# Kernel optimization log

Hardware: AMD Instinct MI355X
Metric: run time of the kernel (lower is better)

Reference implementation:

```python
import jax, jax.numpy as jnp
import numpy as np

D_MODEL = 1024
N_HEADS = 16
D_HEAD = D_MODEL // N_HEADS
LN_EPS = 1e-5


def setup_inputs() -> dict:
    key = jax.random.key(0)
    ks = jax.random.split(key, 8)
    B, T = 4, 2048
    s = 1.0 / np.sqrt(D_MODEL)
    return {
        "encoder_seq": jax.random.normal(ks[0], (B, T, D_MODEL), jnp.float32),
        "decoder_seq": jax.random.normal(ks[1], (B, T, D_MODEL), jnp.float32),
        "Wq": jax.random.normal(ks[2], (D_MODEL, D_MODEL), jnp.float32) * s,
        "bq": jnp.zeros((D_MODEL,), jnp.float32),
        "Wk": jax.random.normal(ks[3], (D_MODEL, D_MODEL), jnp.float32) * s,
        "bk": jnp.zeros((D_MODEL,), jnp.float32),
        "Wv": jax.random.normal(ks[4], (D_MODEL, D_MODEL), jnp.float32) * s,
        "bv": jnp.zeros((D_MODEL,), jnp.float32),
        "ln_gamma": jnp.ones((D_MODEL,), jnp.float32),
        "ln_beta": jnp.zeros((D_MODEL,), jnp.float32),
    }


def layer_norm(x, gamma, beta):
    mu = jnp.mean(x, axis=-1, keepdims=True)
    var = jnp.mean(jnp.square(x - mu), axis=-1, keepdims=True)
    return (x - mu) * jax.lax.rsqrt(var + LN_EPS) * gamma + beta


def reference(encoder_seq, decoder_seq, Wq, bq, Wk, bk, Wv, bv, ln_gamma, ln_beta):
    B, T_dec, _ = decoder_seq.shape
    T_enc = encoder_seq.shape[1]
    # projections (torch Linear: x @ W^T + b)
    q = (decoder_seq @ Wq.T + bq).reshape(B, T_dec, N_HEADS, D_HEAD)
    k = (encoder_seq @ Wk.T + bk).reshape(B, T_enc, N_HEADS, D_HEAD)
    v = (encoder_seq @ Wv.T + bv).reshape(B, T_enc, N_HEADS, D_HEAD)
    scale = 1.0 / np.sqrt(D_HEAD)
    # softmax-free attention: scale*(Q K^T) V == scale * Q (K^T V); avoid [T_dec,T_enc]
    kv = jnp.einsum("bthd,bthe->bhde", k, v)          # [B,H,dh,dh]
    att = jnp.einsum("bqhd,bhde->bqhe", q, kv) * scale  # [B,T_dec,H,dh]
    att = att.reshape(B, T_dec, D_MODEL)
    # dropout is identity in eval mode; residual + LayerNorm
    return layer_norm(att + decoder_seq, ln_gamma, ln_beta)
```

## Files before the change

### kernel.cpp

```cpp
#include <hip/hip_runtime.h>
#include <hip/hip_bf16.h>
#include <stdint.h>
#include <stddef.h>

typedef __attribute__((ext_vector_type(8))) __bf16 bf16x8;
typedef __attribute__((ext_vector_type(4))) float f32x4;

#define DMODEL 1024
#define HEADS  16
#define BATCH  4
#define TSEQ   2048
#define MROWS  (BATCH * TSEQ)
#define NE     (MROWS * DMODEL)
#define NW     (DMODEL * DMODEL)

#define MiB (size_t)1048576
#define QB_OFF   ((size_t)0)
#define KB_OFF   (16 * MiB)
#define VB_OFF   (32 * MiB)
#define ENC_OFF  (48 * MiB)
#define DEC_OFF  (64 * MiB)
#define KVP_OFF  (64 * MiB)
#define WB_OFF   (80 * MiB)
#define KVT_OFF  (86 * MiB)

__global__ __launch_bounds__(256)
void conv_all(const float* __restrict__ enc, const float* __restrict__ dec,
              const float* __restrict__ Wq, const float* __restrict__ Wk,
              const float* __restrict__ Wv,
              __bf16* __restrict__ encB, __bf16* __restrict__ decB,
              __bf16* __restrict__ WB)
{
    const int i = (blockIdx.x * 256 + threadIdx.x) * 8;
    const float* src;
    __bf16* dst;
    int off;
    if (i < NE)            { src = enc; dst = encB; off = i; }
    else if (i < 2 * NE)   { src = dec; dst = decB; off = i - NE; }
    else {
        const int j = i - 2 * NE;
        const int sel = j >> 20;
        off = j & (NW - 1);
        src = (sel == 0) ? Wq : (sel == 1) ? Wk : Wv;
        dst = WB + (size_t)sel * NW;
    }
    f32x4 a = *(const f32x4*)(src + off);
    f32x4 b = *(const f32x4*)(src + off + 4);
    bf16x8 o;
#pragma unroll
    for (int j = 0; j < 4; ++j) { o[j] = (__bf16)a[j]; o[j + 4] = (__bf16)b[j]; }
    *(bf16x8*)(dst + off) = o;
}

__device__ __forceinline__ bf16x8 frag(const __bf16* reg, int rowl, int kh, int g4)
{
    const int slot = ((kh << 2) + g4) ^ (rowl & 7);
    return *(const bf16x8*)(reg + rowl * 64 + slot * 8);
}

__device__ __forceinline__ void stage_half(const __bf16* gbase, int kt,
                                           __bf16* reg, int tid)
{
#pragma unroll
    for (int p = 0; p < 2; ++p) {
        const int c = tid + p * 512;
        const int row = c >> 3, slot = c & 7;
        const __bf16* src = gbase + (size_t)row * DMODEL + kt * 64
                            + ((slot ^ (row & 7)) << 3);
        __builtin_amdgcn_global_load_lds(
            (const __attribute__((address_space(1))) void*)src,
            (__attribute__((address_space(3))) void*)(reg + c * 8), 16, 0, 0);
    }
}

#define VMW(N)  asm volatile("s_waitcnt vmcnt(" #N ")" ::: "memory")
#define LGKM0() asm volatile("s_waitcnt lgkmcnt(0)" ::: "memory")

#define KPHASE(PAR, STAGE_CODE, WAIT_CODE)                                    \
  {                                                                           \
    bf16x8 af[4][2], bfv[4][2];                                               \
    _Pragma("unroll") for (int mf = 0; mf < 4; ++mf)                          \
      _Pragma("unroll") for (int kh = 0; kh < 2; ++kh)                        \
        af[mf][kh] = frag(&ldsA[PAR][0], wm * 64 + mf * 16 + l4, kh, g4);     \
    _Pragma("unroll") for (int nf = 0; nf < 4; ++nf)                          \
      _Pragma("unroll") for (int kh = 0; kh < 2; ++kh)                        \
        bfv[nf][kh] = frag(&ldsB[PAR][bh][0], (wn & 1) * 64 + nf * 16 + l4, kh, g4); \
    LGKM0();                                                                  \
    __builtin_amdgcn_sched_barrier(0);                                        \
    __builtin_amdgcn_s_barrier();        \
    STAGE_CODE;                      \
    __builtin_amdgcn_sched_barrier(0);                                        \
    __builtin_amdgcn_s_setprio(1);                                            \
    _Pragma("unroll") for (int mf = 0; mf < 4; ++mf)                          \
      _Pragma("unroll") for (int nf = 0; nf < 4; ++nf)                        \
        _Pragma("unroll") for (int kh = 0; kh < 2; ++kh)                      \
          acc[mf][nf] = __builtin_amdgcn_mfma_f32_16x16x32_bf16(              \
              af[mf][kh], bfv[nf][kh], acc[mf][nf], 0, 0, 0);                 \
    __builtin_amdgcn_s_setprio(0);                                            \
    WAIT_CODE;                                                                \
    __builtin_amdgcn_s_barrier();    \
  }

__global__ __launch_bounds__(512, 2)
void qkv_gemm(const __bf16* __restrict__ decB, const __bf16* __restrict__ encB,
              const __bf16* __restrict__ WB,
              const float* __restrict__ bq, const float* __restrict__ bk,
              const float* __restrict__ bv,
              __bf16* __restrict__ Qb, __bf16* __restrict__ Kb,
              __bf16* __restrict__ Vb)
{
    __shared__ __align__(16) __bf16 ldsA[2][8192];
    __shared__ __align__(16) __bf16 ldsB[2][2][8192];

    const int tid  = threadIdx.x;
    const int lane = tid & 63;
    const int wv   = tid >> 6;
    const int wm   = wv >> 2;
    const int wn   = wv & 3;
    const int bh   = wn >> 1;
    const int l4   = lane & 15;
    const int g4   = lane >> 4;

    const int bid  = blockIdx.x;
    const int slab = bid & 7;
    const int idx  = bid >> 3;
    const int r    = idx >> 3;
    const int sel  = r >> 2;
    const int bn   = r & 3;
    const int bm   = slab * 8 + (idx & 7);

    const __bf16* A    = (sel == 0) ? decB : encB;
    const __bf16* W    = WB + (size_t)sel * NW;
    const float*  bias = (sel == 0) ? bq : (sel == 1) ? bk : bv;
    __bf16*       C    = (sel == 0) ? Qb : (sel == 1) ? Kb : Vb;

    const __bf16* Ab = A + (size_t)(bm * 128) * DMODEL;
    const __bf16* Wb = W + (size_t)(bn * 256) * DMODEL;

    auto stage_tile = [&](int par, int kt) {
        stage_half(Ab,                        kt, &ldsA[par][0],    tid);
        stage_half(Wb,                        kt, &ldsB[par][0][0], tid);
        stage_half(Wb + (size_t)128 * DMODEL, kt, &ldsB[par][1][0], tid);
    };

    f32x4 acc[4][4] = {};

    stage_tile(0, 0);
    stage_tile(1, 1);
    VMW(6);
    __builtin_amdgcn_s_barrier();

    for (int i = 0; i < 8; ++i) {
        KPHASE(0, { if (i < 7) stage_tile(0, 2 * i + 2); },
                  { if (i < 7) { VMW(6); } else { VMW(0); } })
        KPHASE(1, { if (i < 7) stage_tile(1, 2 * i + 3); },
                  { if (i < 7) { VMW(6); } else { VMW(0); } })
    }

#pragma unroll
    for (int mf = 0; mf < 4; ++mf)
#pragma unroll
        for (int nf = 0; nf < 4; ++nf) {
            const int gm0 = bm * 128 + wm * 64 + mf * 16 + g4 * 4;
            const int gn  = bn * 256 + wn * 64 + nf * 16 + l4;
            const float bv2 = bias[gn];
#pragma unroll
            for (int j = 0; j < 4; ++j)
                C[(size_t)(gm0 + j) * DMODEL + gn] =
                    (__bf16)(acc[mf][nf][j] + bv2);
        }
}

__global__ __launch_bounds__(256)
void kv_mm(const __bf16* __restrict__ Kb, const __bf16* __restrict__ Vb,
           float* __restrict__ kvp)
{
    __shared__ __align__(16) float Ks[128][64];
    __shared__ __align__(16) float Vs[128][64];

    const int tid = threadIdx.x;
    const int bh  = blockIdx.x;
    const int ch  = blockIdx.y;
    const int b   = bh >> 4, h = bh & 15;
    const int w   = tid >> 6, lane = tid & 63;
    const int dg  = (lane >> 3) * 8;
    const int eg  = (lane & 7) * 8;
    const size_t base = (size_t)b * TSEQ + (size_t)ch * 512;

    f32x4 acc[8][2] = {};

    for (int ss = 0; ss < 4; ++ss) {
        __syncthreads();
#pragma unroll
        for (int i = 0; i < 4; ++i) {
            const int e = i * 2048 + tid * 8;
            const int t = e >> 6, d = e & 63;
            bf16x8 k8 = *(const bf16x8*)&Kb[(base + ss * 128 + t) * DMODEL + h * 64 + d];
            bf16x8 v8 = *(const bf16x8*)&Vb[(base + ss * 128 + t) * DMODEL + h * 64 + d];
            f32x4 kf0, kf1, vf0, vf1;
#pragma unroll
            for (int j = 0; j < 4; ++j) {
                kf0[j] = (float)k8[j]; kf1[j] = (float)k8[j + 4];
                vf0[j] = (float)v8[j]; vf1[j] = (float)v8[j + 4];
            }
            *(f32x4*)&Ks[t][d]     = kf0;
            *(f32x4*)&Ks[t][d + 4] = kf1;
            *(f32x4*)&Vs[t][d]     = vf0;
            *(f32x4*)&Vs[t][d + 4] = vf1;
        }
        __syncthreads();

#pragma unroll 4
        for (int tt = 0; tt < 32; ++tt) {
            const int t = w * 32 + tt;
            f32x4 kd0 = *(const f32x4*)&Ks[t][dg];
            f32x4 kd1 = *(const f32x4*)&Ks[t][dg + 4];
            f32x4 ve0 = *(const f32x4*)&Vs[t][eg];
            f32x4 ve1 = *(const f32x4*)&Vs[t][eg + 4];
#pragma unroll
            for (int rr = 0; rr < 8; ++rr) {
                const float kd = (rr < 4) ? kd0[rr] : kd1[rr - 4];
                acc[rr][0] += ve0 * kd;
                acc[rr][1] += ve1 * kd;
            }
        }
    }

    float* o = kvp + ((size_t)(ch * 4 + w) * 64 + bh) * 4096 + (size_t)dg * 64 + eg;
#pragma unroll
    for (int rr = 0; rr < 8; ++rr) {
        *(f32x4*)(o + rr * 64)     = acc[rr][0];
        *(f32x4*)(o + rr * 64 + 4) = acc[rr][1];
    }
}

__global__ __launch_bounds__(256)
void kv_reduce(const float* __restrict__ kvp, __bf16* __restrict__ kvT)
{
    const int idx = blockIdx.x * 256 + threadIdx.x;
    const int bh  = idx >> 12;
    const int rem = idx & 4095;
    const int d = rem >> 6, e = rem & 63;
    float s = 0.f;
#pragma unroll
    for (int c = 0; c < 16; ++c) s += kvp[((size_t)c * 64 + bh) * 4096 + rem];
    kvT[(size_t)bh * 4096 + e * 64 + d] = (__bf16)(s * 0.125f);
}

__global__ __launch_bounds__(256)
void att_ln(const __bf16* __restrict__ Q, const __bf16* __restrict__ kvT,
            const float* __restrict__ dec, const float* __restrict__ gamma,
            const float* __restrict__ beta, float* __restrict__ out)
{
    __shared__ __align__(16) __bf16 att_s[32][1032];

    const int tid  = threadIdx.x;
    const int lane = tid & 63;
    const int w    = tid >> 6;
    const int l4   = lane & 15, g4 = lane >> 4;
    const int t0   = blockIdx.x * 32;
    const int b    = t0 >> 11;

#pragma unroll
    for (int i = 0; i < 4; ++i) {
        const int h = w * 4 + i;
        f32x4 acc[2][4] = {};
#pragma unroll
        for (int kk = 0; kk < 2; ++kk) {
            bf16x8 a0 = *(const bf16x8*)&Q[(size_t)(t0 + l4) * DMODEL + h * 64 + kk * 32 + g4 * 8];
            bf16x8 a1 = *(const bf16x8*)&Q[(size_t)(t0 + 16 + l4) * DMODEL + h * 64 + kk * 32 + g4 * 8];
#pragma unroll
            for (int n = 0; n < 4; ++n) {
                bf16x8 bb = *(const bf16x8*)&kvT[(size_t)(b * 16 + h) * 4096 + (n * 16 + l4) * 64 + kk * 32 + g4 * 8];
                acc[0][n] = __builtin_amdgcn_mfma_f32_16x16x32_bf16(a0, bb, acc[0][n], 0, 0, 0);
                acc[1][n] = __builtin_amdgcn_mfma_f32_16x16x32_bf16(a1, bb, acc[1][n], 0, 0, 0);
            }
        }
#pragma unroll
        for (int m = 0; m < 2; ++m)
#pragma unroll
            for (int n = 0; n < 4; ++n)
#pragma unroll
                for (int j = 0; j < 4; ++j)
                    att_s[m * 16 + g4 * 4 + j][h * 64 + n * 16 + l4] = (__bf16)acc[m][n][j];
    }
    __syncthreads();

    const int rr = tid >> 3, seg = tid & 7;
    const size_t grow = (size_t)t0 + rr;
    float sum = 0.f, ss2 = 0.f;
#pragma unroll
    for (int i = 0; i < 16; ++i) {
        const int c0 = seg * 8 + i * 64;
        bf16x8 av = *(const bf16x8*)&att_s[rr][c0];
        f32x4 d0 = *(const f32x4*)&dec[grow * DMODEL + c0];
        f32x4 d1 = *(const f32x4*)&dec[grow * DMODEL + c0 + 4];
        bf16x8 xs;
#pragma unroll
        for (int j = 0; j < 4; ++j) {
            const float x0 = (float)av[j] + d0[j];
            const float x1 = (float)av[j + 4] + d1[j];
            sum += x0 + x1; ss2 += x0 * x0 + x1 * x1;
            xs[j] = (__bf16)x0; xs[j + 4] = (__bf16)x1;
        }
        *(bf16x8*)&att_s[rr][c0] = xs;
    }
    sum += __shfl_xor(sum, 1); ss2 += __shfl_xor(ss2, 1);
    sum += __shfl_xor(sum, 2); ss2 += __shfl_xor(ss2, 2);
    sum += __shfl_xor(sum, 4); ss2 += __shfl_xor(ss2, 4);
    const float mu   = sum * (1.f / 1024.f);
    const float var  = ss2 * (1.f / 1024.f) - mu * mu;
    const float rstd = rsqrtf(var + 1e-5f);

#pragma unroll
    for (int i = 0; i < 16; ++i) {
        const int c0 = seg * 8 + i * 64;
        bf16x8 xv = *(const bf16x8*)&att_s[rr][c0];
        f32x4 g0 = *(const f32x4*)&gamma[c0];
        f32x4 g1 = *(const f32x4*)&gamma[c0 + 4];
        f32x4 b0 = *(const f32x4*)&beta[c0];
        f32x4 b1 = *(const f32x4*)&beta[c0 + 4];
        f32x4 y0, y1;
#pragma unroll
        for (int j = 0; j < 4; ++j) {
            y0[j] = ((float)xv[j]     - mu) * rstd * g0[j] + b0[j];
            y1[j] = ((float)xv[j + 4] - mu) * rstd * g1[j] + b1[j];
        }
        *(f32x4*)&out[grow * DMODEL + c0]     = y0;
        *(f32x4*)&out[grow * DMODEL + c0 + 4] = y1;
    }
}

extern "C" void kernel_launch(void* const* d_in, const int* in_sizes, int n_in,
                              void* d_out, int out_size, void* d_ws, size_t ws_size,
                              hipStream_t stream)
{
    const float* enc   = (const float*)d_in[0];
    const float* dec   = (const float*)d_in[1];
    const float* Wq    = (const float*)d_in[2];
    const float* bq    = (const float*)d_in[3];
    const float* Wk    = (const float*)d_in[4];
    const float* bk    = (const float*)d_in[5];
    const float* Wv    = (const float*)d_in[6];
    const float* bv    = (const float*)d_in[7];
    const float* gamma = (const float*)d_in[8];
    const float* beta  = (const float*)d_in[9];

    char* ws = (char*)d_ws;
    __bf16* Qb   = (__bf16*)(ws + QB_OFF);
    __bf16* Kb   = (__bf16*)(ws + KB_OFF);
    __bf16* Vb   = (__bf16*)(ws + VB_OFF);
    __bf16* encB = (__bf16*)(ws + ENC_OFF);
    __bf16* decB = (__bf16*)(ws + DEC_OFF);
    float*  kvp  = (float*) (ws + KVP_OFF);
    __bf16* WB   = (__bf16*)(ws + WB_OFF);
    __bf16* kvT  = (__bf16*)(ws + KVT_OFF);

    conv_all<<<9728, 256, 0, stream>>>(enc, dec, Wq, Wk, Wv, encB, decB, WB);
    qkv_gemm<<<768, 512, 0, stream>>>(decB, encB, WB, bq, bk, bv, Qb, Kb, Vb);
    kv_mm<<<dim3(64, 4), 256, 0, stream>>>(Kb, Vb, kvp);
    kv_reduce<<<1024, 256, 0, stream>>>(kvp, kvT);
    att_ln<<<256, 256, 0, stream>>>(Qb, kvT, dec, gamma, beta, (float*)d_out);
}
```

Baseline: 129.8 us.

## Restructure QKV GEMM to 4 waves with 128x64 warp tiles and triple-buffered LDS

The QKV projection GEMM drops from 8 waves to 4 waves per 128x256 block. Each wave now computes a 128x64 output tile with 32 accumulators, which raises register use and MFMA work per fragment load. The double-buffered ping-pong is replaced by a three-slot LDS ring that prefetches two k-tiles ahead, and there is only one barrier per k-step. This aims to cut LDS fragment traffic and barrier overhead, at the cost of lower occupancy (launch bounds 256,1) and larger LDS use (144 KB), so fewer waves are available to hide latency.

Measured after the change: 132.3 us. Within noise of the previous version (+1.9%).

```diff
diff --git a/kernel.cpp b/kernel.cpp
--- a/kernel.cpp
+++ b/kernel.cpp
@@ -58,12 +58,12 @@
     return *(const bf16x8*)(reg + rowl * 64 + slot * 8);
 }
 
-__device__ __forceinline__ void stage_half(const __bf16* gbase, int kt,
-                                           __bf16* reg, int tid)
-{
-#pragma unroll
-    for (int p = 0; p < 2; ++p) {
-        const int c = tid + p * 512;
+__device__ __forceinline__ void stage_half256(const __bf16* gbase, int kt,
+                                              __bf16* reg, int tid)
+{
+#pragma unroll
+    for (int p = 0; p < 4; ++p) {
+        const int c = tid + p * 256;
         const int row = c >> 3, slot = c & 7;
         const __bf16* src = gbase + (size_t)row * DMODEL + kt * 64
                             + ((slot ^ (row & 7)) << 3);
@@ -74,34 +74,8 @@
 }
 
 #define VMW(N)  asm volatile("s_waitcnt vmcnt(" #N ")" ::: "memory")
-#define LGKM0() asm volatile("s_waitcnt lgkmcnt(0)" ::: "memory")
-
-#define KPHASE(PAR, STAGE_CODE, WAIT_CODE)                                    \
-  {                                                                           \
-    bf16x8 af[4][2], bfv[4][2];                                               \
-    _Pragma("unroll") for (int mf = 0; mf < 4; ++mf)                          \
-      _Pragma("unroll") for (int kh = 0; kh < 2; ++kh)                        \
-        af[mf][kh] = frag(&ldsA[PAR][0], wm * 64 + mf * 16 + l4, kh, g4);     \
-    _Pragma("unroll") for (int nf = 0; nf < 4; ++nf)                          \
-      _Pragma("unroll") for (int kh = 0; kh < 2; ++kh)                        \
-        bfv[nf][kh] = frag(&ldsB[PAR][bh][0], (wn & 1) * 64 + nf * 16 + l4, kh, g4); \
-    LGKM0();                                                                  \
-    __builtin_amdgcn_sched_barrier(0);                                        \
-    __builtin_amdgcn_s_barrier();        \
-    STAGE_CODE;                      \
-    __builtin_amdgcn_sched_barrier(0);                                        \
-    __builtin_amdgcn_s_setprio(1);                                            \
-    _Pragma("unroll") for (int mf = 0; mf < 4; ++mf)                          \
-      _Pragma("unroll") for (int nf = 0; nf < 4; ++nf)                        \
-        _Pragma("unroll") for (int kh = 0; kh < 2; ++kh)                      \
-          acc[mf][nf] = __builtin_amdgcn_mfma_f32_16x16x32_bf16(              \
-              af[mf][kh], bfv[nf][kh], acc[mf][nf], 0, 0, 0);                 \
-    __builtin_amdgcn_s_setprio(0);                                            \
-    WAIT_CODE;                                                                \
-    __builtin_amdgcn_s_barrier();    \
-  }
-
-__global__ __launch_bounds__(512, 2)
+
+__global__ __launch_bounds__(256, 1)
 void qkv_gemm(const __bf16* __restrict__ decB, const __bf16* __restrict__ encB,
               const __bf16* __restrict__ WB,
               const float* __restrict__ bq, const float* __restrict__ bk,
@@ -109,15 +83,13 @@
               __bf16* __restrict__ Qb, __bf16* __restrict__ Kb,
               __bf16* __restrict__ Vb)
 {
-    __shared__ __align__(16) __bf16 ldsA[2][8192];
-    __shared__ __align__(16) __bf16 ldsB[2][2][8192];
+    __shared__ __align__(16) __bf16 ldsA[3 * 8192];
+    __shared__ __align__(16) __bf16 ldsB[3 * 16384];
 
     const int tid  = threadIdx.x;
     const int lane = tid & 63;
-    const int wv   = tid >> 6;
-    const int wm   = wv >> 2;
-    const int wn   = wv & 3;
-    const int bh   = wn >> 1;
+    const int wn   = tid >> 6;
+    const int bh2  = wn >> 1;
     const int l4   = lane & 15;
     const int g4   = lane >> 4;
 
@@ -137,31 +109,63 @@
     const __bf16* Ab = A + (size_t)(bm * 128) * DMODEL;
     const __bf16* Wb = W + (size_t)(bn * 256) * DMODEL;
 
-    auto stage_tile = [&](int par, int kt) {
-        stage_half(Ab,                        kt, &ldsA[par][0],    tid);
-        stage_half(Wb,                        kt, &ldsB[par][0][0], tid);
-        stage_half(Wb + (size_t)128 * DMODEL, kt, &ldsB[par][1][0], tid);
+    auto stage_tile = [&](int buf, int kt) {
+        stage_half256(Ab,                        kt, ldsA + buf * 8192,          tid);
+        stage_half256(Wb,                        kt, ldsB + buf * 16384,         tid);
+        stage_half256(Wb + (size_t)128 * DMODEL, kt, ldsB + buf * 16384 + 8192,  tid);
     };
 
-    f32x4 acc[4][4] = {};
+    f32x4 acc[8][4] = {};
 
     stage_tile(0, 0);
     stage_tile(1, 1);
-    VMW(6);
+    VMW(12);
+    __builtin_amdgcn_sched_barrier(0);
     __builtin_amdgcn_s_barrier();
 
-    for (int i = 0; i < 8; ++i) {
-        KPHASE(0, { if (i < 7) stage_tile(0, 2 * i + 2); },
-                  { if (i < 7) { VMW(6); } else { VMW(0); } })
-        KPHASE(1, { if (i < 7) stage_tile(1, 2 * i + 3); },
-                  { if (i < 7) { VMW(6); } else { VMW(0); } })
-    }
-
-#pragma unroll
-    for (int mf = 0; mf < 4; ++mf)
+    int rd = 0, st = 2;
+#pragma unroll 1
+    for (int t = 0; t < 16; ++t) {
+        const __bf16* bA = ldsA + rd * 8192;
+        const __bf16* bB = ldsB + rd * 16384 + bh2 * 8192;
+
+        bf16x8 af[8][2], bf[4][2];
+#pragma unroll
+        for (int mf = 0; mf < 8; ++mf)
+#pragma unroll
+            for (int kh = 0; kh < 2; ++kh)
+                af[mf][kh] = frag(bA, mf * 16 + l4, kh, g4);
+#pragma unroll
+        for (int nf = 0; nf < 4; ++nf)
+#pragma unroll
+            for (int kh = 0; kh < 2; ++kh)
+                bf[nf][kh] = frag(bB, (wn & 1) * 64 + nf * 16 + l4, kh, g4);
+
+        if (t < 14) stage_tile(st, t + 2);
+
+#pragma unroll
+        for (int mf = 0; mf < 8; ++mf)
+#pragma unroll
+            for (int nf = 0; nf < 4; ++nf)
+#pragma unroll
+                for (int kh = 0; kh < 2; ++kh)
+                    acc[mf][nf] = __builtin_amdgcn_mfma_f32_16x16x32_bf16(
+                        af[mf][kh], bf[nf][kh], acc[mf][nf], 0, 0, 0);
+
+        if (t < 14)      { VMW(12); }
+        else if (t == 14){ VMW(0);  }
+        __builtin_amdgcn_sched_barrier(0);
+        __builtin_amdgcn_s_barrier();
+
+        rd = (rd == 2) ? 0 : rd + 1;
+        st = (st == 2) ? 0 : st + 1;
+    }
+
+#pragma unroll
+    for (int mf = 0; mf < 8; ++mf)
 #pragma unroll
         for (int nf = 0; nf < 4; ++nf) {
-            const int gm0 = bm * 128 + wm * 64 + mf * 16 + g4 * 4;
+            const int gm0 = bm * 128 + mf * 16 + g4 * 4;
             const int gn  = bn * 256 + wn * 64 + nf * 16 + l4;
             const float bv2 = bias[gn];
 #pragma unroll
@@ -357,7 +361,7 @@
     __bf16* kvT  = (__bf16*)(ws + KVT_OFF);
 
     conv_all<<<9728, 256, 0, stream>>>(enc, dec, Wq, Wk, Wv, encB, decB, WB);
-    qkv_gemm<<<768, 512, 0, stream>>>(decB, encB, WB, bq, bk, bv, Qb, Kb, Vb);
+    qkv_gemm<<<768, 256, 0, stream>>>(decB, encB, WB, bq, bk, bv, Qb, Kb, Vb);
     kv_mm<<<dim3(64, 4), 256, 0, stream>>>(Kb, Vb, kvp);
     kv_reduce<<<1024, 256, 0, stream>>>(kvp, kvT);
     att_ln<<<256, 256, 0, stream>>>(Qb, kvT, dec, gamma, beta, (float*)d_out);
```

## Reduce kv partials in LDS and read bf16 decoder residual in att_ln

Applied to the files above, without the earlier changes.

kv_mm now sums its four per-wave partial KV products through shared memory before writing, so it stores 4 partials per (batch, head) instead of 16. kv_reduce then reads 4 chunks instead of 16. att_ln reads the decoder residual from the existing bf16 copy instead of fp32, halving that read but lowering residual precision. The kvp buffer moves to overlap encB so the bf16 decoder copy stays live, and the qkv_gemm LDS arrays are flattened with an extra sched_barrier.

After: 123.4 us (median of 2 runs). 1.05x faster.

```diff
diff --git a/kernel.cpp b/kernel.cpp
--- a/kernel.cpp
+++ b/kernel.cpp
@@ -19,8 +19,8 @@
 #define KB_OFF   (16 * MiB)
 #define VB_OFF   (32 * MiB)
 #define ENC_OFF  (48 * MiB)
+#define KVP_OFF  (48 * MiB)
 #define DEC_OFF  (64 * MiB)
-#define KVP_OFF  (64 * MiB)
 #define WB_OFF   (80 * MiB)
 #define KVT_OFF  (86 * MiB)
 
@@ -81,14 +81,15 @@
     bf16x8 af[4][2], bfv[4][2];                                               \
     _Pragma("unroll") for (int mf = 0; mf < 4; ++mf)                          \
       _Pragma("unroll") for (int kh = 0; kh < 2; ++kh)                        \
-        af[mf][kh] = frag(&ldsA[PAR][0], wm * 64 + mf * 16 + l4, kh, g4);     \
+        af[mf][kh] = frag(&ldsA[(PAR) * 8192], wm * 64 + mf * 16 + l4, kh, g4); \
     _Pragma("unroll") for (int nf = 0; nf < 4; ++nf)                          \
       _Pragma("unroll") for (int kh = 0; kh < 2; ++kh)                        \
-        bfv[nf][kh] = frag(&ldsB[PAR][bh][0], (wn & 1) * 64 + nf * 16 + l4, kh, g4); \
+        bfv[nf][kh] = frag(&ldsB[(PAR) * 16384 + bh2 * 8192],                 \
+                           (wn & 1) * 64 + nf * 16 + l4, kh, g4);             \
     LGKM0();                                                                  \
     __builtin_amdgcn_sched_barrier(0);                                        \
-    __builtin_amdgcn_s_barrier();        \
-    STAGE_CODE;                      \
+    __builtin_amdgcn_s_barrier();                                             \
+    STAGE_CODE;                                                               \
     __builtin_amdgcn_sched_barrier(0);                                        \
     __builtin_amdgcn_s_setprio(1);                                            \
     _Pragma("unroll") for (int mf = 0; mf < 4; ++mf)                          \
@@ -98,7 +99,7 @@
               af[mf][kh], bfv[nf][kh], acc[mf][nf], 0, 0, 0);                 \
     __builtin_amdgcn_s_setprio(0);                                            \
     WAIT_CODE;                                                                \
-    __builtin_amdgcn_s_barrier();    \
+    __builtin_amdgcn_s_barrier();                                             \
   }
 
 __global__ __launch_bounds__(512, 2)
@@ -109,15 +110,15 @@
               __bf16* __restrict__ Qb, __bf16* __restrict__ Kb,
               __bf16* __restrict__ Vb)
 {
-    __shared__ __align__(16) __bf16 ldsA[2][8192];
-    __shared__ __align__(16) __bf16 ldsB[2][2][8192];
+    __shared__ __align__(16) __bf16 ldsA[2 * 8192];
+    __shared__ __align__(16) __bf16 ldsB[2 * 16384];
 
     const int tid  = threadIdx.x;
     const int lane = tid & 63;
     const int wv   = tid >> 6;
     const int wm   = wv >> 2;
     const int wn   = wv & 3;
-    const int bh   = wn >> 1;
+    const int bh2  = wn >> 1;
     const int l4   = lane & 15;
     const int g4   = lane >> 4;
 
@@ -130,17 +131,16 @@
     const int bm   = slab * 8 + (idx & 7);
 
     const __bf16* A    = (sel == 0) ? decB : encB;
-    const __bf16* W    = WB + (size_t)sel * NW;
+    const __bf16* Wb   = WB + (size_t)sel * NW + (size_t)(bn * 256) * DMODEL;
     const float*  bias = (sel == 0) ? bq : (sel == 1) ? bk : bv;
     __bf16*       C    = (sel == 0) ? Qb : (sel == 1) ? Kb : Vb;
 
     const __bf16* Ab = A + (size_t)(bm * 128) * DMODEL;
-    const __bf16* Wb = W + (size_t)(bn * 256) * DMODEL;
 
     auto stage_tile = [&](int par, int kt) {
-        stage_half(Ab,                        kt, &ldsA[par][0],    tid);
-        stage_half(Wb,                        kt, &ldsB[par][0][0], tid);
-        stage_half(Wb + (size_t)128 * DMODEL, kt, &ldsB[par][1][0], tid);
+        stage_half(Ab,                        kt, ldsA + par * 8192,         tid);
+        stage_half(Wb,                        kt, ldsB + par * 16384,        tid);
+        stage_half(Wb + (size_t)128 * DMODEL, kt, ldsB + par * 16384 + 8192, tid);
     };
 
     f32x4 acc[4][4] = {};
@@ -148,6 +148,7 @@
     stage_tile(0, 0);
     stage_tile(1, 1);
     VMW(6);
+    __builtin_amdgcn_sched_barrier(0);
     __builtin_amdgcn_s_barrier();
 
     for (int i = 0; i < 8; ++i) {
@@ -226,11 +227,45 @@
         }
     }
 
-    float* o = kvp + ((size_t)(ch * 4 + w) * 64 + bh) * 4096 + (size_t)dg * 64 + eg;
-#pragma unroll
-    for (int rr = 0; rr < 8; ++rr) {
-        *(f32x4*)(o + rr * 64)     = acc[rr][0];
-        *(f32x4*)(o + rr * 64 + 4) = acc[rr][1];
+    float* red = &Ks[0][0];
+    __syncthreads();
+    if (w >= 2) {
+        float* dstw = red + (w - 2) * 4096 + dg * 64 + eg;
+#pragma unroll
+        for (int rr = 0; rr < 8; ++rr) {
+            *(f32x4*)(dstw + rr * 64)     = acc[rr][0];
+            *(f32x4*)(dstw + rr * 64 + 4) = acc[rr][1];
+        }
+    }
+    __syncthreads();
+    if (w < 2) {
+        const float* srcw = red + w * 4096 + dg * 64 + eg;
+#pragma unroll
+        for (int rr = 0; rr < 8; ++rr) {
+            acc[rr][0] += *(const f32x4*)(srcw + rr * 64);
+            acc[rr][1] += *(const f32x4*)(srcw + rr * 64 + 4);
+        }
+    }
+    __syncthreads();
+    if (w == 1) {
+        float* dstw = red + dg * 64 + eg;
+#pragma unroll
+        for (int rr = 0; rr < 8; ++rr) {
+            *(f32x4*)(dstw + rr * 64)     = acc[rr][0];
+            *(f32x4*)(dstw + rr * 64 + 4) = acc[rr][1];
+        }
+    }
+    __syncthreads();
+    if (w == 0) {
+        const float* srcw = red + dg * 64 + eg;
+        float* o = kvp + ((size_t)ch * 64 + bh) * 4096 + (size_t)dg * 64 + eg;
+#pragma unroll
+        for (int rr = 0; rr < 8; ++rr) {
+            f32x4 s0 = acc[rr][0] + *(const f32x4*)(srcw + rr * 64);
+            f32x4 s1 = acc[rr][1] + *(const f32x4*)(srcw + rr * 64 + 4);
+            *(f32x4*)(o + rr * 64)     = s0;
+            *(f32x4*)(o + rr * 64 + 4) = s1;
+        }
     }
 }
 
@@ -243,13 +278,13 @@
     const int d = rem >> 6, e = rem & 63;
     float s = 0.f;
 #pragma unroll
-    for (int c = 0; c < 16; ++c) s += kvp[((size_t)c * 64 + bh) * 4096 + rem];
+    for (int c = 0; c < 4; ++c) s += kvp[((size_t)c * 64 + bh) * 4096 + rem];
     kvT[(size_t)bh * 4096 + e * 64 + d] = (__bf16)(s * 0.125f);
 }
 
 __global__ __launch_bounds__(256)
 void att_ln(const __bf16* __restrict__ Q, const __bf16* __restrict__ kvT,
-            const float* __restrict__ dec, const float* __restrict__ gamma,
+            const __bf16* __restrict__ decB, const float* __restrict__ gamma,
             const float* __restrict__ beta, float* __restrict__ out)
 {
     __shared__ __align__(16) __bf16 att_s[32][1032];
@@ -293,15 +328,13 @@
     for (int i = 0; i < 16; ++i) {
         const int c0 = seg * 8 + i * 64;
         bf16x8 av = *(const bf16x8*)&att_s[rr][c0];
-        f32x4 d0 = *(const f32x4*)&dec[grow * DMODEL + c0];
-        f32x4 d1 = *(const f32x4*)&dec[grow * DMODEL + c0 + 4];
+        bf16x8 dv = *(const bf16x8*)&decB[grow * DMODEL + c0];
         bf16x8 xs;
 #pragma unroll
-        for (int j = 0; j < 4; ++j) {
-            const float x0 = (float)av[j] + d0[j];
-            const float x1 = (float)av[j + 4] + d1[j];
-            sum += x0 + x1; ss2 += x0 * x0 + x1 * x1;
-            xs[j] = (__bf16)x0; xs[j + 4] = (__bf16)x1;
+        for (int j = 0; j < 8; ++j) {
+            const float x = (float)av[j] + (float)dv[j];
+            sum += x; ss2 += x * x;
+            xs[j] = (__bf16)x;
         }
         *(bf16x8*)&att_s[rr][c0] = xs;
     }
@@ -351,8 +384,8 @@
     __bf16* Kb   = (__bf16*)(ws + KB_OFF);
     __bf16* Vb   = (__bf16*)(ws + VB_OFF);
     __bf16* encB = (__bf16*)(ws + ENC_OFF);
+    float*  kvp  = (float*) (ws + KVP_OFF);
     __bf16* decB = (__bf16*)(ws + DEC_OFF);
-    float*  kvp  = (float*) (ws + KVP_OFF);
     __bf16* WB   = (__bf16*)(ws + WB_OFF);
     __bf16* kvT  = (__bf16*)(ws + KVT_OFF);
 
@@ -360,5 +393,5 @@
     qkv_gemm<<<768, 512, 0, stream>>>(decB, encB, WB, bq, bk, bv, Qb, Kb, Vb);
     kv_mm<<<dim3(64, 4), 256, 0, stream>>>(Kb, Vb, kvp);
     kv_reduce<<<1024, 256, 0, stream>>>(kvp, kvT);
-    att_ln<<<256, 256, 0, stream>>>(Qb, kvT, dec, gamma, beta, (float*)d_out);
-}
+    att_ln<<<256, 256, 0, stream>>>(Qb, kvT, decB, gamma, beta, (float*)d_out);
+}
```
